# Performance work log

Hardware: AMD Instinct MI355X
Metric: run time of the kernel (lower is better)

## Reference

```python
import jax, jax.numpy as jnp
import numpy as np

GAMMA = 0.1
NEG = -1e10
BIG = 1e10


def _logsumexp3(a, b, c):
    m = jnp.maximum(jnp.maximum(a, b), c)
    return m + jnp.log(jnp.exp(a - m) + jnp.exp(b - m) + jnp.exp(c - m))


def ctc_loss(log_probs, targets, input_lengths, target_lengths, blank=0):
    """torch.nn.CTCLoss (reduction='mean') on batch-first log_probs (B,T,V)."""
    B, T, V = log_probs.shape
    S = targets.shape[1]
    L = 2 * S + 1
    # extended label sequence: blank, y1, blank, y2, ..., blank
    ext = jnp.full((B, L), blank, targets.dtype).at[:, 1::2].set(targets)
    diff = jnp.concatenate([jnp.zeros((B, 2), bool), ext[:, 2:] != ext[:, :-2]], axis=1)
    skip_ok = (ext != blank) & diff  # (B,L) allow s-2 transition
    lp_t = jnp.transpose(log_probs, (1, 0, 2))  # (T,B,V)

    g0 = jnp.take_along_axis(lp_t[0], ext, axis=1)  # (B,L)
    alpha0 = jnp.where(jnp.arange(L)[None, :] < 2, g0, NEG)

    def step(alpha, inp):
        lp, t = inp
        g = jnp.take_along_axis(lp, ext, axis=1)  # (B,L)
        a1 = alpha
        a2 = jnp.pad(alpha[:, :-1], ((0, 0), (1, 0)), constant_values=NEG)
        a3 = jnp.where(skip_ok, jnp.pad(alpha[:, :-2], ((0, 0), (2, 0)), constant_values=NEG), NEG)
        new = _logsumexp3(a1, a2, a3) + g
        alpha = jnp.where((t < input_lengths)[:, None], new, alpha)  # freeze past length
        return alpha, None

    alpha, _ = jax.lax.scan(step, alpha0, (lp_t[1:], jnp.arange(1, T)))
    l = 2 * target_lengths + 1
    a_last = jnp.take_along_axis(alpha, (l - 1)[:, None], axis=1)[:, 0]
    a_prev = jnp.take_along_axis(alpha, (l - 2)[:, None], axis=1)[:, 0]
    m = jnp.maximum(a_last, a_prev)
    log_lik = m + jnp.log(jnp.exp(a_last - m) + jnp.exp(a_prev - m))
    return jnp.mean(-log_lik / target_lengths.astype(log_probs.dtype))


def soft_dtw(pred, targ, gamma=GAMMA):
    """SoftDTW with squared-L2 cost (pysdtw default). pred (B,T,D), targ (B,S,D)."""
    sq = lambda x: jnp.sum(x * x, -1)
    Dmat = sq(pred)[:, :, None] + sq(targ)[:, None, :] - 2.0 * jnp.einsum('btd,bsd->bts', pred, targ)
    B, T, S = Dmat.shape

    def softmin(a, b, c):
        z = jnp.stack([a, b, c]) * (-1.0 / gamma)
        m = jnp.max(z, 0)
        return -gamma * (m + jnp.log(jnp.sum(jnp.exp(z - m), 0)))

    def row_step(prev, d_row):  # prev: R[i-1, 0..S] (B,S+1); d_row (B,S)
        up = prev[:, 1:].T      # (S,B)
        diag = prev[:, :-1].T

        def col_step(left, inp):
            d, u, dg = inp
            r = d + softmin(u, left, dg)
            return r, r

        _, row = jax.lax.scan(col_step, jnp.full((B,), BIG, Dmat.dtype), (d_row.T, up, diag))
        new = jnp.concatenate([jnp.full((B, 1), BIG, Dmat.dtype), row.T], axis=1)
        return new, None

    init = jnp.concatenate([jnp.zeros((B, 1), Dmat.dtype), jnp.full((B, S), BIG, Dmat.dtype)], axis=1)
    final, _ = jax.lax.scan(row_step, init, jnp.transpose(Dmat, (1, 0, 2)))
    return final[:, -1]  # R[T,S] per batch element


def setup_inputs() -> dict:
    key = jax.random.key(0)
    k1, k2, k3, k4, k5 = jax.random.split(key, 5)
    B, T, V, S, D = 64, 1024, 256, 256, 24
    log_probs = jax.nn.log_softmax(jax.random.normal(k1, (B, T, V), jnp.float32), axis=-1)
    feature_matrix = jax.random.normal(k2, (V, D), jnp.float32)
    targets = jax.random.randint(k3, (B, S), 1, V, jnp.int32)  # labels exclude blank=0
    input_lengths = jax.random.randint(k4, (B,), 768, T + 1, jnp.int32)
    target_lengths = jax.random.randint(k5, (B,), 128, S + 1, jnp.int32)
    return {"log_probs": log_probs, "feature_matrix": feature_matrix, "targets": targets,
            "input_lengths": input_lengths, "target_lengths": target_lengths}


def reference(log_probs, feature_matrix, targets, input_lengths, target_lengths):
    ctc = ctc_loss(log_probs, targets, input_lengths, target_lengths, blank=0)
    probs = jnp.exp(log_probs)                       # (B,T,V)
    predicted_features = probs @ feature_matrix      # (B,T,D)
    target_features = feature_matrix[targets]        # (B,S,D) embedding
    sdtw_loss = jnp.mean(soft_dtw(predicted_features, target_features, GAMMA))
    return ctc + sdtw_loss
```

## Files before the change

### kernel.cpp

```cpp
#include <hip/hip_runtime.h>
#include <math.h>

constexpr int NB = 64;
constexpr int NT = 1024;
constexpr int NV = 256;
constexpr int NS = 256;
constexpr int NL = 2 * NS + 1;
constexpr int NDG = NT + NS - 1;
__device__ constexpr float BIGV = 1e10f;

using f32x4 = __attribute__((ext_vector_type(4))) float;
using s16x8 = __attribute__((ext_vector_type(8))) short;

__device__ __forceinline__ float dpp_shr1_f32(float x, float lane0val) {
    int r = __builtin_amdgcn_update_dpp(__float_as_int(lane0val),
                                        __float_as_int(x), 0x138, 0xf, 0xf, false);
    return __int_as_float(r);
}
__device__ __forceinline__ double dpp_shr1_zero_f64(double x) {
    union { double d; unsigned long long u; } c; c.d = x;
    int lo = (int)(c.u & 0xffffffffull), hi = (int)(c.u >> 32);
    int nlo = __builtin_amdgcn_update_dpp(0, lo, 0x138, 0xf, 0xf, true);
    int nhi = __builtin_amdgcn_update_dpp(0, hi, 0x138, 0xf, 0xf, true);
    c.u = ((unsigned long long)(unsigned)nhi << 32) | (unsigned)nlo;
    return c.d;
}
__device__ __forceinline__ int wave_imax_dpp(int x) {
    int t;
    t = __builtin_amdgcn_update_dpp(0, x, 0x111, 0xf, 0xf, true); x = max(x, t);
    t = __builtin_amdgcn_update_dpp(0, x, 0x112, 0xf, 0xf, true); x = max(x, t);
    t = __builtin_amdgcn_update_dpp(0, x, 0x114, 0xf, 0xf, true); x = max(x, t);
    t = __builtin_amdgcn_update_dpp(0, x, 0x118, 0xf, 0xf, true); x = max(x, t);
    t = __builtin_amdgcn_update_dpp(0, x, 0x142, 0xf, 0xf, true); x = max(x, t);
    t = __builtin_amdgcn_update_dpp(0, x, 0x143, 0xf, 0xf, true); x = max(x, t);
    return __builtin_amdgcn_readlane(x, 63);
}
__device__ __forceinline__ float row16_sum(float x) {
    x += __int_as_float(__builtin_amdgcn_update_dpp(0, __float_as_int(x), 0x111, 0xf, 0xf, true));
    x += __int_as_float(__builtin_amdgcn_update_dpp(0, __float_as_int(x), 0x112, 0xf, 0xf, true));
    x += __int_as_float(__builtin_amdgcn_update_dpp(0, __float_as_int(x), 0x114, 0xf, 0xf, true));
    x += __int_as_float(__builtin_amdgcn_update_dpp(0, __float_as_int(x), 0x118, 0xf, 0xf, true));
    return x;
}
__device__ __forceinline__ unsigned short f2bf(float x) {
    unsigned u = __float_as_uint(x);
    return (unsigned short)((u + 0x7fffu + ((u >> 16) & 1u)) >> 16);
}
__device__ __forceinline__ float bf2f(unsigned short h) {
    return __uint_as_float((unsigned)h << 16);
}

__global__ __launch_bounds__(512, 1) void k_dmat(
    const float* __restrict__ lp, const float* __restrict__ fm,
    const int* __restrict__ tgt, unsigned short* __restrict__ Ddiag,
    unsigned short* __restrict__ Gbf, float* __restrict__ PB)
{
    constexpr int ESTR = 264;
    constexpr int FSTR = 264;
    constexpr int TSTR = 40;
    constexpr int PSTR = 40;
    constexpr int DSTR = 130;

    __shared__ __align__(16) unsigned char uni[128 * ESTR * 2];
    __shared__ __align__(16) unsigned short FT[32 * FSTR];
    __shared__ __align__(16) unsigned short tgf[256 * TSTR];
    __shared__ __align__(16) unsigned short pb16[128 * PSTR];
    __shared__ float tsq[256];
    __shared__ float psq[128];

    unsigned short* E = (unsigned short*)uni;
    float* Dst = (float*)uni;

    const int tid  = threadIdx.x;
    const int lane = tid & 63;
    const int w    = tid >> 6;
    const int b    = blockIdx.x >> 3;
    const int a0   = (blockIdx.x & 7) * 128;

    const int row2 = tid >> 1;
    const int half = tid & 1;
    const int k0   = half * 12;

    {
        const float* fr = fm + row2 * 24 + k0;
        #pragma unroll
        for (int k = 0; k < 12; k += 4) {
            float4 t4 = *(const float4*)(fr + k);
            FT[(k0 + k + 0) * FSTR + row2] = f2bf(t4.x);
            FT[(k0 + k + 1) * FSTR + row2] = f2bf(t4.y);
            FT[(k0 + k + 2) * FSTR + row2] = f2bf(t4.z);
            FT[(k0 + k + 3) * FSTR + row2] = f2bf(t4.w);
        }
        if (half) {
            #pragma unroll
            for (int n = 24; n < 32; ++n) FT[n * FSTR + row2] = 0;
        }
    }
    {
        const int lab_r = tgt[b * NS + row2];
        const float* fr = fm + lab_r * 24 + k0;
        float s = 0.f;
        #pragma unroll
        for (int k = 0; k < 12; k += 4) {
            float4 t4 = *(const float4*)(fr + k);
            unsigned p0 = f2bf(t4.x) | ((unsigned)f2bf(t4.y) << 16);
            unsigned p1 = f2bf(t4.z) | ((unsigned)f2bf(t4.w) << 16);
            *(unsigned*)&tgf[row2 * TSTR + k0 + k]     = p0;
            *(unsigned*)&tgf[row2 * TSTR + k0 + k + 2] = p1;
            s += t4.x * t4.x + t4.y * t4.y + t4.z * t4.z + t4.w * t4.w;
        }
        const float sf = s + __shfl_xor(s, 1);
        if (!half) tsq[row2] = sf;
        else {
            #pragma unroll
            for (int k = 24; k < 32; k += 2) *(unsigned*)&tgf[row2 * TSTR + k] = 0;
        }
    }
    const int lab2 = tgt[b * NS + (tid & 255)];
    {
        const float* src = lp + ((size_t)b * NT + a0) * NV;
        #pragma unroll
        for (int it = 0; it < 16; ++it) {
            int f4  = it * 512 + tid;
            int row = f4 >> 6;
            int c4  = f4 & 63;
            float4 v = *(const float4*)(src + row * NV + c4 * 4);
            float e0 = __expf(v.x), e1 = __expf(v.y);
            float e2 = __expf(v.z), e3 = __expf(v.w);
            unsigned* dst = (unsigned*)&E[row * ESTR + c4 * 4];
            dst[0] = f2bf(e0) | ((unsigned)f2bf(e1) << 16);
            dst[1] = f2bf(e2) | ((unsigned)f2bf(e3) << 16);
            if (c4 == 0) PB[b * NT + a0 + row] = e0;
        }
    }
    __syncthreads();

    {
        unsigned short* gd = Gbf + (((size_t)(b * NT + a0)) << 8) + (tid & 255);
        const int rbit = tid >> 8;
        #pragma unroll 8
        for (int i = 0; i < 64; ++i) {
            int rr = (i << 1) | rbit;
            gd[(size_t)rr << 8] = E[rr * ESTR + lab2];
        }
    }

    const int m0  = 16 * w;
    const int q   = lane >> 4;
    const int n16 = lane & 15;
    f32x4 acc00 = {0.f, 0.f, 0.f, 0.f}, acc01 = acc00;
    #pragma unroll
    for (int ks = 0; ks < 8; ++ks) {
        s16x8 a0f = *(const s16x8*)&E[(m0 + n16) * ESTR + ks * 32 + q * 8];
        s16x8 b0f = *(const s16x8*)&FT[(n16) * FSTR + ks * 32 + q * 8];
        s16x8 b1f = *(const s16x8*)&FT[(16 + n16) * FSTR + ks * 32 + q * 8];
        acc00 = __builtin_amdgcn_mfma_f32_16x16x32_bf16(a0f, b0f, acc00, 0, 0, 0);
        acc01 = __builtin_amdgcn_mfma_f32_16x16x32_bf16(a0f, b1f, acc01, 0, 0, 0);
    }
    #pragma unroll
    for (int r = 0; r < 4; ++r) {
        float s0 = acc00[r] * acc00[r] + acc01[r] * acc01[r];
        s0 = row16_sum(s0);
        if (n16 == 15) psq[m0 + 4 * q + r] = s0;
        pb16[(m0 + 4 * q + r) * PSTR + n16]      = f2bf(acc00[r]);
        pb16[(m0 + 4 * q + r) * PSTR + 16 + n16] = f2bf(acc01[r]);
    }

    #pragma unroll 1
    for (int h = 0; h < 2; ++h) {
        __syncthreads();
        s16x8 pa0 = *(const s16x8*)&pb16[(m0 + n16) * PSTR + q * 8];
        float ps0[4];
        #pragma unroll
        for (int r = 0; r < 4; ++r) ps0[r] = psq[m0 + 4 * q + r];
        #pragma unroll
        for (int nt = 0; nt < 8; ++nt) {
            const int j0 = 16 * nt;
            s16x8 tb = *(const s16x8*)&tgf[(128 * h + j0 + n16) * TSTR + q * 8];
            float tq = tsq[128 * h + j0 + n16];
            f32x4 z = {0.f, 0.f, 0.f, 0.f};
            f32x4 d0 = __builtin_amdgcn_mfma_f32_16x16x32_bf16(pa0, tb, z, 0, 0, 0);
            #pragma unroll
            for (int r = 0; r < 4; ++r)
                Dst[(m0 + 4 * q + r) * DSTR + j0 + n16] = ps0[r] + tq - 2.f * d0[r];
        }
        __syncthreads();
        const size_t dbase = ((size_t)b * NDG + a0 + 128 * h) * NS + 128 * h;
        #pragma unroll 4
        for (int i = 0; i < 32; ++i) {
            int dp  = 8 * i + w;
            int jlo = dp > 127 ? dp - 127 : 0;
            int jhi = dp < 127 ? dp : 127;
            #pragma unroll
            for (int c = 0; c < 2; ++c) {
                int jj = jlo + 64 * c + lane;
                if (jj <= jhi) {
                    unsigned short vv = f2bf(Dst[(dp - jj) * DSTR + jj]);
                    Ddiag[dbase + (size_t)dp * NS + jj] = vv;
                }
            }
        }
    }
}

__global__ __launch_bounds__(64, 1) void k_dp(
    const float* __restrict__ lp, const int* __restrict__ tgt,
    const int* __restrict__ ilen, const int* __restrict__ tlen,
    const unsigned short* __restrict__ Ddiag, const unsigned short* __restrict__ Gbf,
    const float* __restrict__ PB, float* __restrict__ ctc_out,
    float* __restrict__ sdtw_out)
{
    __shared__ double smd[513];
    const int lane = threadIdx.x;
    const int bid = blockIdx.x;

    if (bid < NB) {
        const int b  = bid;
        const int len = ilen[b];
        const int tl  = tlen[b];
        const float* lpb = lp + (size_t)b * NT * NV;
        const unsigned short* Gb = Gbf + ((size_t)(b * NT) << 8);
        const float* PBb = PB + b * NT;

        const int4 t4 = ((const int4*)(tgt + b * NS))[lane];
        const int prevw = __shfl_up(t4.w, 1);
        const double m1d = ((lane > 0) && (t4.x != prevw)) ? 1.0 : 0.0;
        const double m3d = (t4.y != t4.x) ? 1.0 : 0.0;
        const double m5d = (t4.z != t4.y) ? 1.0 : 0.0;
        const double m7d = (t4.w != t4.z) ? 1.0 : 0.0;

        double a0 = 0.0, a1 = 0.0, a2 = 0.0, a3 = 0.0, a4 = 0.0,
               a5 = 0.0, a6 = 0.0, a7 = 0.0, a8 = 0.0;
        if (lane == 0) {
            a0 = (double)__expf(lpb[0]);
            a1 = (double)__expf(lpb[t4.x]);
        }
        long long Ksum = 0;

        auto ctc_step = [&](const ushort4 gu, const float pbf) {
            const double pb = (double)pbf;
            const double p0 = (double)bf2f(gu.x), p1 = (double)bf2f(gu.y);
            const double p2 = (double)bf2f(gu.z), p3 = (double)bf2f(gu.w);
            const double l7 = dpp_shr1_zero_f64(a7);
            const double n0 = (a0 + l7) * pb;
            const double n1 = fma(m1d, l7, a1 + a0) * p0;
            const double n2 = (a2 + a1) * pb;
            const double n3 = fma(m3d, a1, a3 + a2) * p1;
            const double n4 = (a4 + a3) * pb;
            const double n5 = fma(m5d, a3, a5 + a4) * p2;
            const double n6 = (a6 + a5) * pb;
            const double n7 = fma(m7d, a5, a7 + a6) * p3;
            const double n8 = (a8 + a7) * pb;
            a0 = n0; a1 = n1; a2 = n2; a3 = n3; a4 = n4;
            a5 = n5; a6 = n6; a7 = n7; a8 = n8;
        };
        auto ctc_rescale = [&]() {
            double m = fmax(a0, a1);
            m = fmax(m, a2); m = fmax(m, a3); m = fmax(m, a4);
            m = fmax(m, a5); m = fmax(m, a6); m = fmax(m, a7);
            m = fmax(m, a8);
            int Eb = (__double2hiint(m) >> 20) & 0x7ff;
            int Ex = wave_imax_dpp(Eb);
            if (Ex < 1) Ex = 1;
            const double inv = __hiloint2double((2046 - Ex) << 20, 0);
            Ksum += (long long)(Ex - 1023);
            a0 *= inv; a1 *= inv; a2 *= inv; a3 *= inv; a4 *= inv;
            a5 *= inv; a6 *= inv; a7 *= inv; a8 *= inv;
        };

        ushort4 gq[32];
        float   pbq[32];
        #pragma unroll
        for (int q = 0; q < 32; ++q) {
            gq[q]  = *(const ushort4*)(Gb + (((size_t)(1 + q)) << 8) + 4 * lane);
            pbq[q] = PBb[1 + q];
        }

        int t0 = 1;
        for (; t0 + 32 <= len; t0 += 32) {
            #pragma unroll
            for (int u = 0; u < 32; ++u) {
                const int t = t0 + u;
                const ushort4 gu = gq[u];
                const float pbf  = pbq[u];
                int tn = t + 32; if (tn > NT - 1) tn = NT - 1;
                gq[u]  = *(const ushort4*)(Gb + (((size_t)tn) << 8) + 4 * lane);
                pbq[u] = PBb[tn];
                ctc_step(gu, pbf);
                if ((u & 7) == 7) ctc_rescale();
            }
        }
        {
            #pragma unroll
            for (int u = 0; u < 32; ++u) {
                if (t0 + u < len) ctc_step(gq[u], pbq[u]);
                if (u == 7 || u == 15 || u == 23) ctc_rescale();
            }
        }

        smd[lane * 8 + 0] = a0; smd[lane * 8 + 1] = a1;
        smd[lane * 8 + 2] = a2; smd[lane * 8 + 3] = a3;
        smd[lane * 8 + 4] = a4; smd[lane * 8 + 5] = a5;
        smd[lane * 8 + 6] = a6; smd[lane * 8 + 7] = a7;
        if (lane == 63) smd[512] = a8;
        __syncthreads();
        if (lane == 0) {
            const int l = 2 * tl + 1;
            const double s = smd[l - 1] + smd[l - 2];
            const double ll = (double)Ksum * 0.6931471805599453 + log(s);
            ctc_out[b] = (float)(-ll / (double)tl);
        }
    } else {
        const int b = bid - NB;
        const unsigned short* Db = Ddiag + (size_t)b * NDG * NS;

        float rp10 = BIGV, rp11 = BIGV, rp12 = BIGV, rp13 = BIGV;
        float rp20 = BIGV, rp21 = BIGV, rp22 = BIGV, rp23 = BIGV;
        if (lane == 0) rp10 = bf2f(Db[0]);

        ushort4 dq[32];
        #pragma unroll
        for (int q = 0; q < 32; ++q)
            dq[q] = *(const ushort4*)(Db + (size_t)(1 + q) * NS + 4 * lane);

        float res = 0.f;
        for (int d0 = 1; d0 < 1279; d0 += 32) {
            #pragma unroll
            for (int u = 0; u < 32; ++u) {
                const int d = d0 + u;
                const ushort4 Dv = dq[u];
                int dn = d + 32; if (dn > NDG - 1) dn = NDG - 1;
                dq[u] = *(const ushort4*)(Db + (size_t)dn * NS + 4 * lane);

                const float Dx = bf2f(Dv.x), Dy = bf2f(Dv.y);
                const float Dz = bf2f(Dv.z), Dw = bf2f(Dv.w);

                const float lf1 = dpp_shr1_f32(rp13, BIGV);
                const float lf2 = dpp_shr1_f32(rp23, BIGV);

                const float c0 = Dx + fminf(fminf(rp10, lf1),  lf2);
                const float c1 = Dy + fminf(fminf(rp11, rp10), rp20);
                const float c2 = Dz + fminf(fminf(rp12, rp11), rp21);
                const float c3 = Dw + fminf(fminf(rp13, rp12), rp22);

                rp20 = rp10; rp21 = rp11; rp22 = rp12; rp23 = rp13;
                rp10 = c0;   rp11 = c1;   rp12 = c2;   rp13 = c3;

                res = (d == NDG - 1) ? c3 : res;
            }
        }
        if (lane == 63) sdtw_out[b] = res;
    }
}

__global__ __launch_bounds__(64) void k_final(
    const float* __restrict__ ctc_out, const float* __restrict__ sdtw_out,
    float* __restrict__ out)
{
    int lane = threadIdx.x;
    float c = ctc_out[lane];
    float s = sdtw_out[lane];
    #pragma unroll
    for (int off = 32; off > 0; off >>= 1) {
        c += __shfl_down(c, off);
        s += __shfl_down(s, off);
    }
    if (lane == 0) out[0] = c / 64.f + s / 64.f;
}

extern "C" void kernel_launch(void* const* d_in, const int* in_sizes, int n_in,
                              void* d_out, int out_size, void* d_ws, size_t ws_size,
                              hipStream_t stream) {
    const float* lp   = (const float*)d_in[0];
    const float* fm   = (const float*)d_in[1];
    const int*   tgt  = (const int*)d_in[2];
    const int*   ilen = (const int*)d_in[3];
    const int*   tlen = (const int*)d_in[4];
    float* out = (float*)d_out;

    char* ws = (char*)d_ws;
    unsigned short* Ddiag = (unsigned short*)ws;
    size_t dbytes = (size_t)NB * NDG * NS * sizeof(unsigned short);
    unsigned short* Gbf = (unsigned short*)(ws + dbytes);
    size_t gbytes = (size_t)NB * NT * NS * sizeof(unsigned short);
    float* PB = (float*)(ws + dbytes + gbytes);
    size_t pbytes = (size_t)NB * NT * sizeof(float);
    float* ctc_res  = (float*)(ws + dbytes + gbytes + pbytes);
    float* sdtw_res = ctc_res + 64;

    hipLaunchKernelGGL(k_dmat, dim3(NB * 8), dim3(512), 0, stream,
                       lp, fm, tgt, Ddiag, Gbf, PB);
    hipLaunchKernelGGL(k_dp, dim3(2 * NB), dim3(64), 0, stream,
                       lp, tgt, ilen, tlen, Ddiag, Gbf, PB, ctc_res, sdtw_res);
    hipLaunchKernelGGL(k_final, dim3(1), dim3(64), 0, stream, ctc_res, sdtw_res, out);
}
```

Baseline: 228.2 us.

## Run CTC recursion alongside distance-matrix kernel, gathering log-probs directly

The CTC alpha recursion moves out of the DP kernel into the first kernel as 64 extra blocks, so it runs concurrently with the distance-matrix blocks instead of waiting for them. It now reads the five needed log-probs per step straight from the input and exponentiates them in-kernel, which removes the intermediate bf16 gathered-probability and blank-probability buffers and their writes. SoftDTW becomes a separate kernel that runs afterwards. The cost is scattered 4-byte global gathers on the serial CTC path with a shallower 8-step prefetch, the CTC blocks occupying 512-thread slots while using only one wave, and the omission of the barrier before reading shared memory, which is safe only within a single wave.

```diff
diff --git a/kernel.cpp b/kernel.cpp
--- a/kernel.cpp
+++ b/kernel.cpp
@@ -50,10 +50,11 @@
     return __uint_as_float((unsigned)h << 16);
 }
 
-__global__ __launch_bounds__(512, 1) void k_dmat(
+__global__ __launch_bounds__(512, 1) void k_main(
     const float* __restrict__ lp, const float* __restrict__ fm,
-    const int* __restrict__ tgt, unsigned short* __restrict__ Ddiag,
-    unsigned short* __restrict__ Gbf, float* __restrict__ PB)
+    const int* __restrict__ tgt, const int* __restrict__ ilen,
+    const int* __restrict__ tlen, unsigned short* __restrict__ Ddiag,
+    float* __restrict__ ctc_out)
 {
     constexpr int ESTR = 264;
     constexpr int FSTR = 264;
@@ -68,159 +69,13 @@
     __shared__ float tsq[256];
     __shared__ float psq[128];
 
-    unsigned short* E = (unsigned short*)uni;
-    float* Dst = (float*)uni;
-
-    const int tid  = threadIdx.x;
-    const int lane = tid & 63;
-    const int w    = tid >> 6;
-    const int b    = blockIdx.x >> 3;
-    const int a0   = (blockIdx.x & 7) * 128;
-
-    const int row2 = tid >> 1;
-    const int half = tid & 1;
-    const int k0   = half * 12;
-
-    {
-        const float* fr = fm + row2 * 24 + k0;
-        #pragma unroll
-        for (int k = 0; k < 12; k += 4) {
-            float4 t4 = *(const float4*)(fr + k);
-            FT[(k0 + k + 0) * FSTR + row2] = f2bf(t4.x);
-            FT[(k0 + k + 1) * FSTR + row2] = f2bf(t4.y);
-            FT[(k0 + k + 2) * FSTR + row2] = f2bf(t4.z);
-            FT[(k0 + k + 3) * FSTR + row2] = f2bf(t4.w);
-        }
-        if (half) {
-            #pragma unroll
-            for (int n = 24; n < 32; ++n) FT[n * FSTR + row2] = 0;
-        }
-    }
-    {
-        const int lab_r = tgt[b * NS + row2];
-        const float* fr = fm + lab_r * 24 + k0;
-        float s = 0.f;
-        #pragma unroll
-        for (int k = 0; k < 12; k += 4) {
-            float4 t4 = *(const float4*)(fr + k);
-            unsigned p0 = f2bf(t4.x) | ((unsigned)f2bf(t4.y) << 16);
-            unsigned p1 = f2bf(t4.z) | ((unsigned)f2bf(t4.w) << 16);
-            *(unsigned*)&tgf[row2 * TSTR + k0 + k]     = p0;
-            *(unsigned*)&tgf[row2 * TSTR + k0 + k + 2] = p1;
-            s += t4.x * t4.x + t4.y * t4.y + t4.z * t4.z + t4.w * t4.w;
-        }
-        const float sf = s + __shfl_xor(s, 1);
-        if (!half) tsq[row2] = sf;
-        else {
-            #pragma unroll
-            for (int k = 24; k < 32; k += 2) *(unsigned*)&tgf[row2 * TSTR + k] = 0;
-        }
-    }
-    const int lab2 = tgt[b * NS + (tid & 255)];
-    {
-        const float* src = lp + ((size_t)b * NT + a0) * NV;
-        #pragma unroll
-        for (int it = 0; it < 16; ++it) {
-            int f4  = it * 512 + tid;
-            int row = f4 >> 6;
-            int c4  = f4 & 63;
-            float4 v = *(const float4*)(src + row * NV + c4 * 4);
-            float e0 = __expf(v.x), e1 = __expf(v.y);
-            float e2 = __expf(v.z), e3 = __expf(v.w);
-            unsigned* dst = (unsigned*)&E[row * ESTR + c4 * 4];
-            dst[0] = f2bf(e0) | ((unsigned)f2bf(e1) << 16);
-            dst[1] = f2bf(e2) | ((unsigned)f2bf(e3) << 16);
-            if (c4 == 0) PB[b * NT + a0 + row] = e0;
-        }
-    }
-    __syncthreads();
-
-    {
-        unsigned short* gd = Gbf + (((size_t)(b * NT + a0)) << 8) + (tid & 255);
-        const int rbit = tid >> 8;
-        #pragma unroll 8
-        for (int i = 0; i < 64; ++i) {
-            int rr = (i << 1) | rbit;
-            gd[(size_t)rr << 8] = E[rr * ESTR + lab2];
-        }
-    }
-
-    const int m0  = 16 * w;
-    const int q   = lane >> 4;
-    const int n16 = lane & 15;
-    f32x4 acc00 = {0.f, 0.f, 0.f, 0.f}, acc01 = acc00;
-    #pragma unroll
-    for (int ks = 0; ks < 8; ++ks) {
-        s16x8 a0f = *(const s16x8*)&E[(m0 + n16) * ESTR + ks * 32 + q * 8];
-        s16x8 b0f = *(const s16x8*)&FT[(n16) * FSTR + ks * 32 + q * 8];
-        s16x8 b1f = *(const s16x8*)&FT[(16 + n16) * FSTR + ks * 32 + q * 8];
-        acc00 = __builtin_amdgcn_mfma_f32_16x16x32_bf16(a0f, b0f, acc00, 0, 0, 0);
-        acc01 = __builtin_amdgcn_mfma_f32_16x16x32_bf16(a0f, b1f, acc01, 0, 0, 0);
-    }
-    #pragma unroll
-    for (int r = 0; r < 4; ++r) {
-        float s0 = acc00[r] * acc00[r] + acc01[r] * acc01[r];
-        s0 = row16_sum(s0);
-        if (n16 == 15) psq[m0 + 4 * q + r] = s0;
-        pb16[(m0 + 4 * q + r) * PSTR + n16]      = f2bf(acc00[r]);
-        pb16[(m0 + 4 * q + r) * PSTR + 16 + n16] = f2bf(acc01[r]);
-    }
-
-    #pragma unroll 1
-    for (int h = 0; h < 2; ++h) {
-        __syncthreads();
-        s16x8 pa0 = *(const s16x8*)&pb16[(m0 + n16) * PSTR + q * 8];
-        float ps0[4];
-        #pragma unroll
-        for (int r = 0; r < 4; ++r) ps0[r] = psq[m0 + 4 * q + r];
-        #pragma unroll
-        for (int nt = 0; nt < 8; ++nt) {
-            const int j0 = 16 * nt;
-            s16x8 tb = *(const s16x8*)&tgf[(128 * h + j0 + n16) * TSTR + q * 8];
-            float tq = tsq[128 * h + j0 + n16];
-            f32x4 z = {0.f, 0.f, 0.f, 0.f};
-            f32x4 d0 = __builtin_amdgcn_mfma_f32_16x16x32_bf16(pa0, tb, z, 0, 0, 0);
-            #pragma unroll
-            for (int r = 0; r < 4; ++r)
-                Dst[(m0 + 4 * q + r) * DSTR + j0 + n16] = ps0[r] + tq - 2.f * d0[r];
-        }
-        __syncthreads();
-        const size_t dbase = ((size_t)b * NDG + a0 + 128 * h) * NS + 128 * h;
-        #pragma unroll 4
-        for (int i = 0; i < 32; ++i) {
-            int dp  = 8 * i + w;
-            int jlo = dp > 127 ? dp - 127 : 0;
-            int jhi = dp < 127 ? dp : 127;
-            #pragma unroll
-            for (int c = 0; c < 2; ++c) {
-                int jj = jlo + 64 * c + lane;
-                if (jj <= jhi) {
-                    unsigned short vv = f2bf(Dst[(dp - jj) * DSTR + jj]);
-                    Ddiag[dbase + (size_t)dp * NS + jj] = vv;
-                }
-            }
-        }
-    }
-}
-
-__global__ __launch_bounds__(64, 1) void k_dp(
-    const float* __restrict__ lp, const int* __restrict__ tgt,
-    const int* __restrict__ ilen, const int* __restrict__ tlen,
-    const unsigned short* __restrict__ Ddiag, const unsigned short* __restrict__ Gbf,
-    const float* __restrict__ PB, float* __restrict__ ctc_out,
-    float* __restrict__ sdtw_out)
-{
-    __shared__ double smd[513];
-    const int lane = threadIdx.x;
-    const int bid = blockIdx.x;
-
-    if (bid < NB) {
-        const int b  = bid;
+    if (blockIdx.x < NB) {
+        if (threadIdx.x >= 64) return;
+        const int lane = threadIdx.x;
+        const int b = blockIdx.x;
         const int len = ilen[b];
         const int tl  = tlen[b];
         const float* lpb = lp + (size_t)b * NT * NV;
-        const unsigned short* Gb = Gbf + ((size_t)(b * NT) << 8);
-        const float* PBb = PB + b * NT;
 
         const int4 t4 = ((const int4*)(tgt + b * NS))[lane];
         const int prevw = __shfl_up(t4.w, 1);
@@ -237,10 +92,10 @@
         }
         long long Ksum = 0;
 
-        auto ctc_step = [&](const ushort4 gu, const float pbf) {
-            const double pb = (double)pbf;
-            const double p0 = (double)bf2f(gu.x), p1 = (double)bf2f(gu.y);
-            const double p2 = (double)bf2f(gu.z), p3 = (double)bf2f(gu.w);
+        auto ctc_step = [&](float f0, float f1, float f2, float f3, float fb) {
+            const double pb = (double)__expf(fb);
+            const double p0 = (double)__expf(f0), p1 = (double)__expf(f1);
+            const double p2 = (double)__expf(f2), p3 = (double)__expf(f3);
             const double l7 = dpp_shr1_zero_f64(a7);
             const double n0 = (a0 + l7) * pb;
             const double n1 = fma(m1d, l7, a1 + a0) * p0;
@@ -268,89 +123,219 @@
             a5 *= inv; a6 *= inv; a7 *= inv; a8 *= inv;
         };
 
-        ushort4 gq[32];
-        float   pbq[32];
-        #pragma unroll
-        for (int q = 0; q < 32; ++q) {
-            gq[q]  = *(const ushort4*)(Gb + (((size_t)(1 + q)) << 8) + 4 * lane);
-            pbq[q] = PBb[1 + q];
+        float q0[8], q1[8], q2[8], q3[8], qb[8];
+        #pragma unroll
+        for (int u = 0; u < 8; ++u) {
+            const float* r = lpb + (size_t)(1 + u) * NV;
+            q0[u] = r[t4.x]; q1[u] = r[t4.y];
+            q2[u] = r[t4.z]; q3[u] = r[t4.w];
+            qb[u] = r[0];
         }
 
         int t0 = 1;
-        for (; t0 + 32 <= len; t0 += 32) {
-            #pragma unroll
-            for (int u = 0; u < 32; ++u) {
-                const int t = t0 + u;
-                const ushort4 gu = gq[u];
-                const float pbf  = pbq[u];
-                int tn = t + 32; if (tn > NT - 1) tn = NT - 1;
-                gq[u]  = *(const ushort4*)(Gb + (((size_t)tn) << 8) + 4 * lane);
-                pbq[u] = PBb[tn];
-                ctc_step(gu, pbf);
-                if ((u & 7) == 7) ctc_rescale();
+        for (; t0 + 8 <= len; t0 += 8) {
+            #pragma unroll
+            for (int u = 0; u < 8; ++u) {
+                const float f0 = q0[u], f1 = q1[u], f2 = q2[u], f3 = q3[u];
+                const float fb = qb[u];
+                int tn = t0 + 8 + u; if (tn > NT - 1) tn = NT - 1;
+                const float* r = lpb + (size_t)tn * NV;
+                q0[u] = r[t4.x]; q1[u] = r[t4.y];
+                q2[u] = r[t4.z]; q3[u] = r[t4.w];
+                qb[u] = r[0];
+                ctc_step(f0, f1, f2, f3, fb);
+                if (u == 7) ctc_rescale();
             }
         }
         {
             #pragma unroll
-            for (int u = 0; u < 32; ++u) {
-                if (t0 + u < len) ctc_step(gq[u], pbq[u]);
-                if (u == 7 || u == 15 || u == 23) ctc_rescale();
+            for (int u = 0; u < 8; ++u) {
+                if (t0 + u < len) ctc_step(q0[u], q1[u], q2[u], q3[u], qb[u]);
             }
         }
 
+        double* smd = (double*)uni;
         smd[lane * 8 + 0] = a0; smd[lane * 8 + 1] = a1;
         smd[lane * 8 + 2] = a2; smd[lane * 8 + 3] = a3;
         smd[lane * 8 + 4] = a4; smd[lane * 8 + 5] = a5;
         smd[lane * 8 + 6] = a6; smd[lane * 8 + 7] = a7;
         if (lane == 63) smd[512] = a8;
-        __syncthreads();
         if (lane == 0) {
             const int l = 2 * tl + 1;
             const double s = smd[l - 1] + smd[l - 2];
             const double ll = (double)Ksum * 0.6931471805599453 + log(s);
             ctc_out[b] = (float)(-ll / (double)tl);
         }
-    } else {
-        const int b = bid - NB;
-        const unsigned short* Db = Ddiag + (size_t)b * NDG * NS;
-
-        float rp10 = BIGV, rp11 = BIGV, rp12 = BIGV, rp13 = BIGV;
-        float rp20 = BIGV, rp21 = BIGV, rp22 = BIGV, rp23 = BIGV;
-        if (lane == 0) rp10 = bf2f(Db[0]);
-
-        ushort4 dq[32];
-        #pragma unroll
-        for (int q = 0; q < 32; ++q)
-            dq[q] = *(const ushort4*)(Db + (size_t)(1 + q) * NS + 4 * lane);
-
-        float res = 0.f;
-        for (int d0 = 1; d0 < 1279; d0 += 32) {
-            #pragma unroll
-            for (int u = 0; u < 32; ++u) {
-                const int d = d0 + u;
-                const ushort4 Dv = dq[u];
-                int dn = d + 32; if (dn > NDG - 1) dn = NDG - 1;
-                dq[u] = *(const ushort4*)(Db + (size_t)dn * NS + 4 * lane);
-
-                const float Dx = bf2f(Dv.x), Dy = bf2f(Dv.y);
-                const float Dz = bf2f(Dv.z), Dw = bf2f(Dv.w);
-
-                const float lf1 = dpp_shr1_f32(rp13, BIGV);
-                const float lf2 = dpp_shr1_f32(rp23, BIGV);
-
-                const float c0 = Dx + fminf(fminf(rp10, lf1),  lf2);
-                const float c1 = Dy + fminf(fminf(rp11, rp10), rp20);
-                const float c2 = Dz + fminf(fminf(rp12, rp11), rp21);
-                const float c3 = Dw + fminf(fminf(rp13, rp12), rp22);
-
-                rp20 = rp10; rp21 = rp11; rp22 = rp12; rp23 = rp13;
-                rp10 = c0;   rp11 = c1;   rp12 = c2;   rp13 = c3;
-
-                res = (d == NDG - 1) ? c3 : res;
+        return;
+    }
+
+    unsigned short* E = (unsigned short*)uni;
+    float* Dst = (float*)uni;
+
+    const int tid  = threadIdx.x;
+    const int lane = tid & 63;
+    const int w    = tid >> 6;
+    const int bb   = blockIdx.x - NB;
+    const int b    = bb >> 3;
+    const int a0   = (bb & 7) * 128;
+
+    const int row2 = tid >> 1;
+    const int half = tid & 1;
+    const int k0   = half * 12;
+
+    {
+        const float* fr = fm + row2 * 24 + k0;
+        #pragma unroll
+        for (int k = 0; k < 12; k += 4) {
+            float4 t4 = *(const float4*)(fr + k);
+            FT[(k0 + k + 0) * FSTR + row2] = f2bf(t4.x);
+            FT[(k0 + k + 1) * FSTR + row2] = f2bf(t4.y);
+            FT[(k0 + k + 2) * FSTR + row2] = f2bf(t4.z);
+            FT[(k0 + k + 3) * FSTR + row2] = f2bf(t4.w);
+        }
+        if (half) {
+            #pragma unroll
+            for (int n = 24; n < 32; ++n) FT[n * FSTR + row2] = 0;
+        }
+    }
+    {
+        const int lab_r = tgt[b * NS + row2];
+        const float* fr = fm + lab_r * 24 + k0;
+        float s = 0.f;
+        #pragma unroll
+        for (int k = 0; k < 12; k += 4) {
+            float4 t4 = *(const float4*)(fr + k);
+            unsigned p0 = f2bf(t4.x) | ((unsigned)f2bf(t4.y) << 16);
+            unsigned p1 = f2bf(t4.z) | ((unsigned)f2bf(t4.w) << 16);
+            *(unsigned*)&tgf[row2 * TSTR + k0 + k]     = p0;
+            *(unsigned*)&tgf[row2 * TSTR + k0 + k + 2] = p1;
+            s += t4.x * t4.x + t4.y * t4.y + t4.z * t4.z + t4.w * t4.w;
+        }
+        const float sf = s + __shfl_xor(s, 1);
+        if (!half) tsq[row2] = sf;
+        else {
+            #pragma unroll
+            for (int k = 24; k < 32; k += 2) *(unsigned*)&tgf[row2 * TSTR + k] = 0;
+        }
+    }
+    {
+        const float* src = lp + ((size_t)b * NT + a0) * NV;
+        #pragma unroll
+        for (int it = 0; it < 16; ++it) {
+            int f4  = it * 512 + tid;
+            int row = f4 >> 6;
+            int c4  = f4 & 63;
+            float4 v = *(const float4*)(src + row * NV + c4 * 4);
+            float e0 = __expf(v.x), e1 = __expf(v.y);
+            float e2 = __expf(v.z), e3 = __expf(v.w);
+            unsigned* dst = (unsigned*)&E[row * ESTR + c4 * 4];
+            dst[0] = f2bf(e0) | ((unsigned)f2bf(e1) << 16);
+            dst[1] = f2bf(e2) | ((unsigned)f2bf(e3) << 16);
+        }
+    }
+    __syncthreads();
+
+    const int m0  = 16 * w;
+    const int q   = lane >> 4;
+    const int n16 = lane & 15;
+    f32x4 acc00 = {0.f, 0.f, 0.f, 0.f}, acc01 = acc00;
+    #pragma unroll
+    for (int ks = 0; ks < 8; ++ks) {
+        s16x8 a0f = *(const s16x8*)&E[(m0 + n16) * ESTR + ks * 32 + q * 8];
+        s16x8 b0f = *(const s16x8*)&FT[(n16) * FSTR + ks * 32 + q * 8];
+        s16x8 b1f = *(const s16x8*)&FT[(16 + n16) * FSTR + ks * 32 + q * 8];
+        acc00 = __builtin_amdgcn_mfma_f32_16x16x32_bf16(a0f, b0f, acc00, 0, 0, 0);
+        acc01 = __builtin_amdgcn_mfma_f32_16x16x32_bf16(a0f, b1f, acc01, 0, 0, 0);
+    }
+    #pragma unroll
+    for (int r = 0; r < 4; ++r) {
+        float s0 = acc00[r] * acc00[r] + acc01[r] * acc01[r];
+        s0 = row16_sum(s0);
+        if (n16 == 15) psq[m0 + 4 * q + r] = s0;
+        pb16[(m0 + 4 * q + r) * PSTR + n16]      = f2bf(acc00[r]);
+        pb16[(m0 + 4 * q + r) * PSTR + 16 + n16] = f2bf(acc01[r]);
+    }
+
+    #pragma unroll 1
+    for (int h = 0; h < 2; ++h) {
+        __syncthreads();
+        s16x8 pa0 = *(const s16x8*)&pb16[(m0 + n16) * PSTR + q * 8];
+        float ps0[4];
+        #pragma unroll
+        for (int r = 0; r < 4; ++r) ps0[r] = psq[m0 + 4 * q + r];
+        #pragma unroll
+        for (int nt = 0; nt < 8; ++nt) {
+            const int j0 = 16 * nt;
+            s16x8 tb = *(const s16x8*)&tgf[(128 * h + j0 + n16) * TSTR + q * 8];
+            float tq = tsq[128 * h + j0 + n16];
+            f32x4 z = {0.f, 0.f, 0.f, 0.f};
+            f32x4 d0 = __builtin_amdgcn_mfma_f32_16x16x32_bf16(pa0, tb, z, 0, 0, 0);
+            #pragma unroll
+            for (int r = 0; r < 4; ++r)
+                Dst[(m0 + 4 * q + r) * DSTR + j0 + n16] = ps0[r] + tq - 2.f * d0[r];
+        }
+        __syncthreads();
+        const size_t dbase = ((size_t)b * NDG + a0 + 128 * h) * NS + 128 * h;
+        #pragma unroll 4
+        for (int i = 0; i < 32; ++i) {
+            int dp  = 8 * i + w;
+            int jlo = dp > 127 ? dp - 127 : 0;
+            int jhi = dp < 127 ? dp : 127;
+            #pragma unroll
+            for (int c = 0; c < 2; ++c) {
+                int jj = jlo + 64 * c + lane;
+                if (jj <= jhi) {
+                    unsigned short vv = f2bf(Dst[(dp - jj) * DSTR + jj]);
+                    Ddiag[dbase + (size_t)dp * NS + jj] = vv;
+                }
             }
         }
-        if (lane == 63) sdtw_out[b] = res;
-    }
+    }
+}
+
+__global__ __launch_bounds__(64, 1) void k_sdtw(
+    const unsigned short* __restrict__ Ddiag, float* __restrict__ sdtw_out)
+{
+    const int lane = threadIdx.x;
+    const int b = blockIdx.x;
+    const unsigned short* Db = Ddiag + (size_t)b * NDG * NS;
+
+    float rp10 = BIGV, rp11 = BIGV, rp12 = BIGV, rp13 = BIGV;
+    float rp20 = BIGV, rp21 = BIGV, rp22 = BIGV, rp23 = BIGV;
+    if (lane == 0) rp10 = bf2f(Db[0]);
+
+    ushort4 dq[32];
+    #pragma unroll
+    for (int q = 0; q < 32; ++q)
+        dq[q] = *(const ushort4*)(Db + (size_t)(1 + q) * NS + 4 * lane);
+
+    float res = 0.f;
+    for (int d0 = 1; d0 < 1279; d0 += 32) {
+        #pragma unroll
+        for (int u = 0; u < 32; ++u) {
+            const int d = d0 + u;
+            const ushort4 Dv = dq[u];
+            int dn = d + 32; if (dn > NDG - 1) dn = NDG - 1;
+            dq[u] = *(const ushort4*)(Db + (size_t)dn * NS + 4 * lane);
+
+            const float Dx = bf2f(Dv.x), Dy = bf2f(Dv.y);
+            const float Dz = bf2f(Dv.z), Dw = bf2f(Dv.w);
+
+            const float lf1 = dpp_shr1_f32(rp13, BIGV);
+            const float lf2 = dpp_shr1_f32(rp23, BIGV);
+
+            const float c0 = Dx + fminf(fminf(rp10, lf1),  lf2);
+            const float c1 = Dy + fminf(fminf(rp11, rp10), rp20);
+            const float c2 = Dz + fminf(fminf(rp12, rp11), rp21);
+            const float c3 = Dw + fminf(fminf(rp13, rp12), rp22);
+
+            rp20 = rp10; rp21 = rp11; rp22 = rp12; rp23 = rp13;
+            rp10 = c0;   rp11 = c1;   rp12 = c2;   rp13 = c3;
+
+            res = (d == NDG - 1) ? c3 : res;
+        }
+    }
+    if (lane == 63) sdtw_out[b] = res;
 }
 
 __global__ __launch_bounds__(64) void k_final(
@@ -381,16 +366,12 @@
     char* ws = (char*)d_ws;
     unsigned short* Ddiag = (unsigned short*)ws;
     size_t dbytes = (size_t)NB * NDG * NS * sizeof(unsigned short);
-    unsigned short* Gbf = (unsigned short*)(ws + dbytes);
-    size_t gbytes = (size_t)NB * NT * NS * sizeof(unsigned short);
-    float* PB = (float*)(ws + dbytes + gbytes);
-    size_t pbytes = (size_t)NB * NT * sizeof(float);
-    float* ctc_res  = (float*)(ws + dbytes + gbytes + pbytes);
+    float* ctc_res  = (float*)(ws + dbytes);
     float* sdtw_res = ctc_res + 64;
 
-    hipLaunchKernelGGL(k_dmat, dim3(NB * 8), dim3(512), 0, stream,
-                       lp, fm, tgt, Ddiag, Gbf, PB);
-    hipLaunchKernelGGL(k_dp, dim3(2 * NB), dim3(64), 0, stream,
-                       lp, tgt, ilen, tlen, Ddiag, Gbf, PB, ctc_res, sdtw_res);
+    hipLaunchKernelGGL(k_main, dim3(NB + NB * 8), dim3(512), 0, stream,
+                       lp, fm, tgt, ilen, tlen, Ddiag, ctc_res);
+    hipLaunchKernelGGL(k_sdtw, dim3(NB), dim3(64), 0, stream,
+                       Ddiag, sdtw_res);
     hipLaunchKernelGGL(k_final, dim3(1), dim3(64), 0, stream, ctc_res, sdtw_res, out);
 }
```

Result: slower. 286.4 us (+25.5%).
